# Kernel tuning notes

Measured on AMD Instinct MI355X. Metric: run time of the kernel, lower is better.

The kernel has to match this reference:

```python
import jax, jax.numpy as jnp
import numpy as np

B, H, W, C = 32, 56, 56, 384
WS, SHIFT, HEADS = 7, 3, 12
HIDDEN = 4 * C
N = WS * WS
HEAD_DIM = C // HEADS
SCALE = HEAD_DIM ** -0.5
EPS = 1e-5


def _rel_index(w):
    coords = np.stack(np.meshgrid(np.arange(w), np.arange(w), indexing='ij'))  # [2,w,w]
    cf = coords.reshape(2, -1)                      # [2, w*w]
    rel = (cf[:, :, None] - cf[:, None, :]).transpose(1, 2, 0)  # [N,N,2]
    rel[:, :, 0] += w - 1
    rel[:, :, 1] += w - 1
    rel[:, :, 0] *= 2 * w - 1
    return rel.sum(-1)                              # [N,N] int

REL_IDX = jnp.asarray(_rel_index(WS))


def _layernorm(x, g, b):
    mu = jnp.mean(x, -1, keepdims=True)
    var = jnp.var(x, -1, keepdims=True)
    return (x - mu) * jax.lax.rsqrt(var + EPS) * g + b


def setup_inputs() -> dict:
    key = jax.random.key(0)
    ks = jax.random.split(key, 10)
    s = 0.02
    return {
        'x': jax.random.normal(ks[0], (B, H * W, C), jnp.float32),
        'norm1_g': jnp.ones((C,), jnp.float32),
        'norm1_b': jnp.zeros((C,), jnp.float32),
        'qkv_w': jax.random.normal(ks[1], (C, 3 * C), jnp.float32) * s,
        'qkv_b': jnp.zeros((3 * C,), jnp.float32),
        'rel_bias': jax.random.normal(ks[2], ((2 * WS - 1) ** 2, HEADS), jnp.float32) * s,
        'proj_w': jax.random.normal(ks[3], (C, C), jnp.float32) * s,
        'proj_b': jnp.zeros((C,), jnp.float32),
        'norm2_g': jnp.ones((C,), jnp.float32),
        'norm2_b': jnp.zeros((C,), jnp.float32),
        'fc1_w': jax.random.normal(ks[4], (C, HIDDEN), jnp.float32) * s,
        'fc1_b': jnp.zeros((HIDDEN,), jnp.float32),
        'fc2_w': jax.random.normal(ks[5], (HIDDEN, C), jnp.float32) * s,
        'fc2_b': jnp.zeros((C,), jnp.float32),
    }


def reference(x, norm1_g, norm1_b, qkv_w, qkv_b, rel_bias, proj_w, proj_b,
              norm2_g, norm2_b, fc1_w, fc1_b, fc2_w, fc2_b):
    shortcut = x
    h = _layernorm(x, norm1_g, norm1_b).reshape(B, H, W, C)
    # shifted windows (H,W divisible by WS -> no padding)
    h = jnp.roll(h, (-SHIFT, -SHIFT), axis=(1, 2))
    nH, nW = H // WS, W // WS
    # window partition: [B*nH*nW, N, C]
    win = h.reshape(B, nH, WS, nW, WS, C).transpose(0, 1, 3, 2, 4, 5).reshape(-1, N, C)
    # window attention (source passes mask=None unconditionally)
    qkv = (win @ qkv_w + qkv_b).reshape(-1, N, 3, HEADS, HEAD_DIM)
    q, k, v = [qkv[:, :, i].transpose(0, 2, 1, 3) for i in range(3)]  # [Bw,h,N,d]
    attn = jnp.einsum('bhnd,bhmd->bhnm', q * SCALE, k)
    bias = rel_bias[REL_IDX.reshape(-1)].reshape(N, N, HEADS).transpose(2, 0, 1)
    attn = jax.nn.softmax(attn + bias[None], axis=-1)
    out = jnp.einsum('bhnm,bhmd->bhnd', attn, v).transpose(0, 2, 1, 3).reshape(-1, N, C)
    out = out @ proj_w + proj_b
    # window reverse + unshift
    h = out.reshape(B, nH, nW, WS, WS, C).transpose(0, 1, 3, 2, 4, 5).reshape(B, H, W, C)
    h = jnp.roll(h, (SHIFT, SHIFT), axis=(1, 2)).reshape(B, H * W, C)
    x = shortcut + h
    # MLP
    m = _layernorm(x, norm2_g, norm2_b)
    m = jax.nn.gelu(m @ fc1_w + fc1_b, approximate=False) @ fc2_w + fc2_b
    return x + m
```

## Files before the change

kernel.cpp:

```cpp
#include <hip/hip_runtime.h>
#include <hip/hip_bf16.h>
#include <math.h>

using bf = __hip_bfloat16;
typedef unsigned short u16;
typedef __attribute__((ext_vector_type(8))) unsigned short us8;
typedef __attribute__((ext_vector_type(8))) __bf16 bf16x8;
typedef __attribute__((ext_vector_type(4))) float f32x4;

static constexpr int kC    = 384;
static constexpr int kHid  = 1536;
static constexpr int kHeads= 12;
static constexpr int kN    = 49;
static constexpr float kScale = 0.17677669529663687f;
static constexpr int kWinsTot = 2048;
static constexpr int kRowsTot = kWinsTot * kN;

__device__ __forceinline__ float b2f(bf v){ return __bfloat162float(v); }
__device__ __forceinline__ bf    f2b(float v){ return __float2bfloat16(v); }
__device__ __forceinline__ float ldf(const float* p){ return *p; }
__device__ __forceinline__ float ldf(const bf* p){ return b2f(*p); }

__device__ __forceinline__ float gelu_f(float v){
  float v2 = v*v;
  float y  = v * (0.7978845608f + 0.0356774081f*v2);
  float e  = __builtin_amdgcn_exp2f(y * 2.885390082f);
  float r  = __builtin_amdgcn_rcpf(1.f + e);
  return v - v*r;
}

__device__ __forceinline__ void gload16(const void* g, void* l){
  __builtin_amdgcn_global_load_lds(
      (const __attribute__((address_space(1))) void*)g,
      (__attribute__((address_space(3))) void*)l, 16, 0, 0);
}

__global__ void tr_k(const float* __restrict__ in, bf* __restrict__ out, int K, int N){
  int i = blockIdx.x*256 + threadIdx.x;
  if (i < K*N){ int k = i / N, n = i - k*N; out[(size_t)n*K + k] = f2b(in[i]); }
}

template<int GATHER, typename TIN>
__global__ __launch_bounds__(256) void ln_k(const TIN* __restrict__ x, const float* __restrict__ g,
                                            const float* __restrict__ be, bf* __restrict__ out,
                                            int winbase){
  int wv = threadIdx.x >> 6, lane = threadIdx.x & 63;
  int lr = blockIdx.x*4 + wv;
  const TIN* src;
  if constexpr (GATHER){
    int win = lr / kN, n = lr - win*kN;
    int gw = winbase + win;
    int b = gw >> 6, rem = gw & 63, wh = rem >> 3, ww = rem & 7;
    int ih = n / 7, iw = n - ih*7;
    int h0 = (wh*7 + ih + 3) % 56;
    int w0 = (ww*7 + iw + 3) % 56;
    src = x + ((size_t)b*3136 + h0*56 + w0) * kC;
  } else {
    src = x + (size_t)lr * kC;
  }
  float vals[6]; float s = 0.f, sq = 0.f;
  #pragma unroll
  for (int j = 0; j < 6; ++j){ float f = ldf(src + j*64 + lane); vals[j] = f; s += f; sq += f*f; }
  #pragma unroll
  for (int o = 32; o > 0; o >>= 1){ s += __shfl_down(s, o); sq += __shfl_down(sq, o); }
  s = __shfl(s, 0); sq = __shfl(sq, 0);
  float mean = s * (1.f/384.f);
  float var  = sq * (1.f/384.f) - mean*mean;
  float rstd = rsqrtf(var + 1e-5f);
  bf* dst = out + (size_t)lr * kC;
  #pragma unroll
  for (int j = 0; j < 6; ++j){
    int c = j*64 + lane;
    dst[c] = f2b((vals[j]-mean)*rstd*g[c] + be[c]);
  }
}

template<int EPI, int ALT = 0>
__global__ __launch_bounds__(256, 3) void gemm_k(const bf* __restrict__ A, const bf* __restrict__ Wt,
                                                 const float* __restrict__ bias, int K, int nbn,
                                                 bf* o0, bf* o1, bf* o2,
                                                 float* fo, const void* res, int aux){
  __shared__ char smem[49152];
  u16 (*sA)[4096] = (u16(*)[4096])smem;
  u16 (*sB)[4096] = (u16(*)[4096])(smem + 24576);
  int nwg = gridDim.x, id = blockIdx.x;
  int q = nwg >> 3, r = nwg & 7, xcd = id & 7, off = id >> 3;
  int swz = (xcd < r ? xcd*(q+1) : r*(q+1) + (xcd-r)*q) + off;
  int bm = (swz / nbn) << 7, bn = (swz % nbn) << 7;

  int t = threadIdx.x, lane = t & 63, wv = t >> 6;
  int scol = ((lane & 3) ^ ((lane >> 3) & 3)) * 8;
  const u16* Ag = (const u16*)A  + (size_t)(bm + wv*32 + (lane >> 2))*K + scol;
  const u16* Bg = (const u16*)Wt + (size_t)(bn + wv*32 + (lane >> 2))*K + scol;
  size_t rstep = (size_t)16 * K;
  int l0 = wv*32*32;

  int wr = wv >> 1, wc = wv & 1, lr = lane & 15, lk = lane >> 4;
  int runit = lk ^ ((lr >> 1) & 3);
  int ro = (wr*64 + lr)*32 + runit*8;
  int co = (wc*64 + lr)*32 + runit*8;
  f32x4 acc[4][4];
  #pragma unroll
  for (int i = 0; i < 4; ++i)
    #pragma unroll
    for (int j = 0; j < 4; ++j) acc[i][j] = (f32x4){0.f,0.f,0.f,0.f};

  int nst = K >> 5;
  #define STG(tt, b) { \
    const u16* ag_ = Ag + (size_t)(tt)*32; const u16* bg_ = Bg + (size_t)(tt)*32; \
    gload16(ag_,         &sA[b][l0]);       gload16(ag_ + rstep, &sA[b][l0 + 512]); \
    gload16(bg_,         &sB[b][l0]);       gload16(bg_ + rstep, &sB[b][l0 + 512]); }
  #define STEP(b, tt) { \
    if ((tt) + 2 < nst)      { asm volatile("s_waitcnt vmcnt(8)" ::: "memory"); } \
    else if ((tt) + 1 < nst) { asm volatile("s_waitcnt vmcnt(4)" ::: "memory"); } \
    else                     { asm volatile("s_waitcnt vmcnt(0)" ::: "memory"); } \
    __builtin_amdgcn_s_barrier(); \
    bf16x8 af[4], bfr[4]; \
    _Pragma("unroll") \
    for (int mi = 0; mi < 4; ++mi) af[mi]  = __builtin_bit_cast(bf16x8, *(const us8*)&sA[b][ro + mi*512]); \
    _Pragma("unroll") \
    for (int ni = 0; ni < 4; ++ni) bfr[ni] = __builtin_bit_cast(bf16x8, *(const us8*)&sB[b][co + ni*512]); \
    __builtin_amdgcn_s_setprio(1); \
    _Pragma("unroll") \
    for (int mi = 0; mi < 4; ++mi) \
      _Pragma("unroll") \
      for (int ni = 0; ni < 4; ++ni) \
        acc[mi][ni] = __builtin_amdgcn_mfma_f32_16x16x32_bf16(af[mi], bfr[ni], acc[mi][ni], 0, 0, 0); \
    __builtin_amdgcn_s_setprio(0); \
    asm volatile("s_waitcnt lgkmcnt(0)" ::: "memory"); \
    __builtin_amdgcn_s_barrier(); \
    if ((tt) + 3 < nst) STG((tt) + 3, b); }

  STG(0, 0); STG(1, 1); STG(2, 2);
  for (int tt = 0; tt < nst; tt += 3){
    STEP(0, tt); STEP(1, tt + 1); STEP(2, tt + 2);
  }
  #undef STEP
  #undef STG

  float* tl = (float*)smem + wv*1088;
  float bs[4];
  #pragma unroll
  for (int ni = 0; ni < 4; ++ni) bs[ni] = bias[bn + wc*64 + ni*16 + lr];
  int rrow = lane >> 2, cb = (lane & 3) * 16;
  int colg = bn + wc*64 + cb;
  #pragma unroll
  for (int mi = 0; mi < 4; ++mi){
    #pragma unroll
    for (int ni = 0; ni < 4; ++ni)
      #pragma unroll
      for (int r2 = 0; r2 < 4; ++r2)
        tl[(lk*4 + r2)*68 + ni*16 + lr] = acc[mi][ni][r2] + bs[ni];
    float vals[16];
    #pragma unroll
    for (int j = 0; j < 16; ++j) vals[j] = tl[rrow*68 + cb + j];
    int row = bm + wr*64 + mi*16 + rrow;
    if constexpr (EPI == 0){
      int which = colg / kC; int cc = colg - which*kC; int hd = cc >> 5, d0 = cc & 31;
      int win = row / kN, n = row - win*kN;
      size_t po = (size_t)(win*kHeads + hd)*2048 + n*32 + d0;
      float sc = which == 0 ? kScale : 1.f;
      bf* dst = which == 0 ? o0 : (which == 1 ? o1 : o2);
      us8 p0, p1;
      #pragma unroll
      for (int j = 0; j < 8; ++j){
        p0[j] = __builtin_bit_cast(u16, f2b(vals[j]   * sc));
        p1[j] = __builtin_bit_cast(u16, f2b(vals[j+8] * sc));
      }
      *(us8*)((u16*)dst + po)     = p0;
      *(us8*)((u16*)dst + po + 8) = p1;
    } else if constexpr (EPI == 1){
      int win = row / kN, n = row - win*kN;
      int gw = aux + win;
      int b = gw >> 6, rem = gw & 63, wh = rem >> 3, ww = rem & 7;
      int ih = n / 7, iw = n - ih*7;
      int h0 = (wh*7 + ih + 3) % 56;
      int w0 = (ww*7 + iw + 3) % 56;
      size_t base = ((size_t)b*3136 + h0*56 + w0)*kC + colg;
      const float* xr = (const float*)res;
      #pragma unroll
      for (int q4 = 0; q4 < 4; ++q4){
        f32x4 rv = *(const f32x4*)(xr + base + q4*4);
        #pragma unroll
        for (int j = 0; j < 4; ++j) vals[q4*4 + j] += rv[j];
      }
      if constexpr (ALT){
        us8 p0, p1;
        #pragma unroll
        for (int j = 0; j < 8; ++j){
          p0[j] = __builtin_bit_cast(u16, f2b(vals[j]));
          p1[j] = __builtin_bit_cast(u16, f2b(vals[j+8]));
        }
        *(us8*)((u16*)o0 + base)     = p0;
        *(us8*)((u16*)o0 + base + 8) = p1;
      } else {
        #pragma unroll
        for (int q4 = 0; q4 < 4; ++q4)
          *(f32x4*)(fo + base + q4*4) = (f32x4){vals[q4*4], vals[q4*4+1], vals[q4*4+2], vals[q4*4+3]};
      }
    } else if constexpr (EPI == 2){
      size_t base = (size_t)row*kHid + colg;
      us8 p0, p1;
      #pragma unroll
      for (int j = 0; j < 16; ++j){
        float v = gelu_f(vals[j]);
        if (j < 8) p0[j] = __builtin_bit_cast(u16, f2b(v));
        else       p1[j-8] = __builtin_bit_cast(u16, f2b(v));
      }
      *(us8*)((u16*)o0 + base)     = p0;
      *(us8*)((u16*)o0 + base + 8) = p1;
    } else {
      size_t base = (size_t)row*kC + colg;
      if constexpr (ALT){
        const u16* xb = (const u16*)res;
        us8 r0 = *(const us8*)(xb + base), r1 = *(const us8*)(xb + base + 8);
        #pragma unroll
        for (int j = 0; j < 8; ++j){
          vals[j]   += b2f(__builtin_bit_cast(bf, (u16)r0[j]));
          vals[j+8] += b2f(__builtin_bit_cast(bf, (u16)r1[j]));
        }
      } else {
        const float* xr = (const float*)res;
        #pragma unroll
        for (int q4 = 0; q4 < 4; ++q4){
          f32x4 rv = *(const f32x4*)(xr + base + q4*4);
          #pragma unroll
          for (int j = 0; j < 4; ++j) vals[q4*4 + j] += rv[j];
        }
      }
      #pragma unroll
      for (int q4 = 0; q4 < 4; ++q4)
        *(f32x4*)(fo + base + q4*4) = (f32x4){vals[q4*4], vals[q4*4+1], vals[q4*4+2], vals[q4*4+3]};
    }
  }
}

__global__ __launch_bounds__(256) void attn_k(const bf* __restrict__ qq, const bf* __restrict__ kk,
                                              const bf* __restrict__ vv, const float* __restrict__ relb,
                                              bf* __restrict__ out){
  __shared__ float rbs[169*kHeads];
  __shared__ u16 plds[4][64*64];
  int t = threadIdx.x, wv = t >> 6, l = t & 63;
  for (int i = t; i < 169*kHeads; i += 256) rbs[i] = relb[i];

  int bid = blockIdx.x*4 + wv, lw = bid / kHeads, h = bid - lw*kHeads;
  const u16* qp = (const u16*)qq + (size_t)bid*2048;
  const u16* kp = (const u16*)kk + (size_t)bid*2048;
  const u16* vp = (const u16*)vv + (size_t)bid*2048;
  int fr = l & 15, fk = l >> 4;

  bf16x8 qf[4], kf[4];
  #pragma unroll
  for (int ti = 0; ti < 4; ++ti){
    qf[ti] = __builtin_bit_cast(bf16x8, *(const us8*)(qp + (ti*16 + fr)*32 + fk*8));
    kf[ti] = __builtin_bit_cast(bf16x8, *(const us8*)(kp + (ti*16 + fr)*32 + fk*8));
  }
  f32x4 s[4][4];
  #pragma unroll
  for (int i = 0; i < 4; ++i)
    #pragma unroll
    for (int j = 0; j < 4; ++j) s[i][j] = (f32x4){0.f,0.f,0.f,0.f};
  #pragma unroll
  for (int ti = 0; ti < 4; ++ti)
    #pragma unroll
    for (int tj = 0; tj < 4; ++tj)
      s[ti][tj] = __builtin_amdgcn_mfma_f32_16x16x32_bf16(qf[ti], kf[tj], s[ti][tj], 0, 0, 0);
  __syncthreads();

  int kh[4], kw[4], cvalid[4];
  #pragma unroll
  for (int tj = 0; tj < 4; ++tj){
    int c = tj*16 + fr;
    kh[tj] = c / 7; kw[tj] = c - kh[tj]*7; cvalid[tj] = c < kN;
  }
  #pragma unroll
  for (int ti = 0; ti < 4; ++ti){
    #pragma unroll
    for (int reg = 0; reg < 4; ++reg){
      int R = ti*16 + fk*4 + reg;
      int Rc = R < kN ? R : kN-1;
      int ih = Rc / 7, iw = Rc - ih*7;
      float v[4];
      #pragma unroll
      for (int tj = 0; tj < 4; ++tj){
        float b = rbs[((ih - kh[tj] + 6)*13 + (iw - kw[tj] + 6))*kHeads + h];
        v[tj] = cvalid[tj] ? s[ti][tj][reg] + b : -1e30f;
      }
      float m = fmaxf(fmaxf(v[0], v[1]), fmaxf(v[2], v[3]));
      #pragma unroll
      for (int msk = 1; msk < 16; msk <<= 1) m = fmaxf(m, __shfl_xor(m, msk));
      float e0 = __expf(v[0]-m), e1 = __expf(v[1]-m), e2 = __expf(v[2]-m), e3 = __expf(v[3]-m);
      float sum = (e0+e1) + (e2+e3);
      #pragma unroll
      for (int msk = 1; msk < 16; msk <<= 1) sum += __shfl_xor(sum, msk);
      float inv = 1.f / sum;
      s[ti][0][reg] = e0*inv; s[ti][1][reg] = e1*inv;
      s[ti][2][reg] = e2*inv; s[ti][3][reg] = e3*inv;
    }
  }
  u16* P = plds[wv];
  #pragma unroll
  for (int ti = 0; ti < 4; ++ti)
    #pragma unroll
    for (int tj = 0; tj < 4; ++tj)
      #pragma unroll
      for (int reg = 0; reg < 4; ++reg){
        int R = ti*16 + fk*4 + reg, c = tj*16 + fr;
        P[R*64 + (((c>>3) ^ (R&7)) << 3) + (c&7)] = __builtin_bit_cast(u16, f2b(s[ti][tj][reg]));
      }
  f32x4 o[4][2];
  #pragma unroll
  for (int i = 0; i < 4; ++i){ o[i][0] = (f32x4){0.f,0.f,0.f,0.f}; o[i][1] = (f32x4){0.f,0.f,0.f,0.f}; }
  #pragma unroll
  for (int ks = 0; ks < 2; ++ks){
    bf16x8 vf[2];
    #pragma unroll
    for (int tdj = 0; tdj < 2; ++tdj){
      us8 tmp;
      #pragma unroll
      for (int j = 0; j < 8; ++j)
        tmp[j] = vp[(ks*32 + fk*8 + j)*32 + tdj*16 + fr];
      vf[tdj] = __builtin_bit_cast(bf16x8, tmp);
    }
    #pragma unroll
    for (int ti = 0; ti < 4; ++ti){
      bf16x8 af = __builtin_bit_cast(bf16x8, *(const us8*)&P[(ti*16 + fr)*64 + (((ks*4 + fk) ^ (fr&7)) << 3)]);
      #pragma unroll
      for (int tdj = 0; tdj < 2; ++tdj)
        o[ti][tdj] = __builtin_amdgcn_mfma_f32_16x16x32_bf16(af, vf[tdj], o[ti][tdj], 0, 0, 0);
    }
  }
  #pragma unroll
  for (int ti = 0; ti < 4; ++ti)
    #pragma unroll
    for (int reg = 0; reg < 4; ++reg){
      int R = ti*16 + fk*4 + reg;
      if (R < kN){
        bf* op = out + ((size_t)lw*kN + R)*kC + h*32;
        #pragma unroll
        for (int tdj = 0; tdj < 2; ++tdj)
          op[tdj*16 + fr] = f2b(o[ti][tdj][reg]);
      }
    }
}

extern "C" void kernel_launch(void* const* d_in, const int* in_sizes, int n_in,
                              void* d_out, int out_size, void* d_ws, size_t ws_size,
                              hipStream_t stream){
  (void)in_sizes; (void)n_in; (void)out_size;
  const float* x     = (const float*)d_in[0];
  const float* n1g   = (const float*)d_in[1];
  const float* n1b   = (const float*)d_in[2];
  const float* qkvw  = (const float*)d_in[3];
  const float* qkvb  = (const float*)d_in[4];
  const float* relb  = (const float*)d_in[5];
  const float* projw = (const float*)d_in[6];
  const float* projb = (const float*)d_in[7];
  const float* n2g   = (const float*)d_in[8];
  const float* n2b   = (const float*)d_in[9];
  const float* fc1w  = (const float*)d_in[10];
  const float* fc1b  = (const float*)d_in[11];
  const float* fc2w  = (const float*)d_in[12];
  const float* fc2b  = (const float*)d_in[13];
  float* out = (float*)d_out;
  char* w = (char*)d_ws;

  const size_t WINB_F = 77070336;
  const size_t BIGB_F = 308281344;
  const size_t WTSB   = 3538944;
  const size_t planeF = (size_t)kWinsTot*kHeads*2048;
  const size_t NEED_M = WINB_F + BIGB_F + WTSB + WINB_F;

  if (ws_size >= NEED_M){
    bf* winbuf = (bf*)w;
    bf* big    = (bf*)(w + WINB_F);
    bf* wts    = (bf*)(w + WINB_F + BIGB_F);
    bf* x1b    = (bf*)(w + WINB_F + BIGB_F + WTSB);
    bf* qkvwt  = wts;
    bf* projwt = qkvwt + 442368;
    bf* fc1wt  = projwt + 147456;
    bf* fc2wt  = fc1wt + 589824;
    bf* qb = big; bf* kb = big + planeF; bf* vb = big + 2*planeF;

    tr_k<<<dim3((442368+255)/256), 256, 0, stream>>>(qkvw,  qkvwt, 384, 1152);
    tr_k<<<dim3((147456+255)/256), 256, 0, stream>>>(projw, projwt, 384, 384);
    tr_k<<<dim3((589824+255)/256), 256, 0, stream>>>(fc1w,  fc1wt, 384, 1536);
    tr_k<<<dim3((589824+255)/256), 256, 0, stream>>>(fc2w,  fc2wt, 1536, 384);

    ln_k<1, float><<<kRowsTot/4, 256, 0, stream>>>(x, n1g, n1b, winbuf, 0);
    gemm_k<0><<<784*9, 256, 0, stream>>>(winbuf, qkvwt, qkvb, 384, 9,
                                         qb, kb, vb, nullptr, nullptr, 0);
    attn_k<<<kWinsTot*kHeads/4, 256, 0, stream>>>(qb, kb, vb, relb, winbuf);
    gemm_k<1,1><<<784*3, 256, 0, stream>>>(winbuf, projwt, projb, 384, 3,
                                           x1b, nullptr, nullptr, nullptr, x, 0);
    ln_k<0, bf><<<kRowsTot/4, 256, 0, stream>>>(x1b, n2g, n2b, winbuf, 0);
    gemm_k<2><<<784*12, 256, 0, stream>>>(winbuf, fc1wt, fc1b, 384, 12,
                                          big, nullptr, nullptr, nullptr, nullptr, 0);
    gemm_k<3,1><<<784*3, 256, 0, stream>>>(big, fc2wt, fc2b, 1536, 3,
                                           nullptr, nullptr, nullptr, out, x1b, 0);
  } else {
    const int cw = 512, crows = cw*kN;
    const size_t WINB = 19267584, BIGB = 77070336;
    const size_t planeC = (size_t)cw*kHeads*2048;
    bf* winbuf = (bf*)w;
    bf* big    = (bf*)(w + WINB);
    bf* wts    = (bf*)(w + WINB + BIGB);
    bf* qkvwt  = wts;
    bf* projwt = qkvwt + 442368;
    bf* fc1wt  = projwt + 147456;
    bf* fc2wt  = fc1wt + 589824;
    bf* qb = big; bf* kb = big + planeC; bf* vb = big + 2*planeC;

    tr_k<<<dim3((442368+255)/256), 256, 0, stream>>>(qkvw,  qkvwt, 384, 1152);
    tr_k<<<dim3((147456+255)/256), 256, 0, stream>>>(projw, projwt, 384, 384);
    tr_k<<<dim3((589824+255)/256), 256, 0, stream>>>(fc1w,  fc1wt, 384, 1536);
    tr_k<<<dim3((589824+255)/256), 256, 0, stream>>>(fc2w,  fc2wt, 1536, 384);

    for (int c = 0; c < 4; ++c){
      int winbase = c * cw;
      ln_k<1, float><<<crows/4, 256, 0, stream>>>(x, n1g, n1b, winbuf, winbase);
      gemm_k<0><<<196*9, 256, 0, stream>>>(winbuf, qkvwt, qkvb, 384, 9,
                                           qb, kb, vb, nullptr, nullptr, 0);
      attn_k<<<cw*kHeads/4, 256, 0, stream>>>(qb, kb, vb, relb, winbuf);
      gemm_k<1,0><<<196*3, 256, 0, stream>>>(winbuf, projwt, projb, 384, 3,
                                             nullptr, nullptr, nullptr, out, x, winbase);
    }
    for (int c = 0; c < 4; ++c){
      float* xr = out + (size_t)c * crows * kC;
      ln_k<0, float><<<crows/4, 256, 0, stream>>>(xr, n2g, n2b, winbuf, 0);
      gemm_k<2><<<196*12, 256, 0, stream>>>(winbuf, fc1wt, fc1b, 384, 12,
                                            big, nullptr, nullptr, nullptr, nullptr, 0);
      gemm_k<3,0><<<196*3, 256, 0, stream>>>(big, fc2wt, fc2b, 1536, 3,
                                             nullptr, nullptr, nullptr, xr, xr, 0);
    }
  }
}
```

Before: 838.5 us.

## Process the fast path in two window chunks to shrink intermediate buffers

The full-workspace path now runs the whole layer pipeline (LN1, QKV GEMM, attention, proj, LN2, FC1, FC2) as two chunks of 1024 windows instead of one pass over all 2048. This halves the window and hidden-activation scratch buffers, so each stage's intermediates are more likely to stay resident in the large last-level cache between kernels rather than going to HBM. It also lowers the workspace needed to take this path. The cost is twice as many kernel launches and half-sized grids per launch.

```diff
diff --git a/kernel.cpp b/kernel.cpp
--- a/kernel.cpp
+++ b/kernel.cpp
@@ -13,8 +13,6 @@
 static constexpr int kHeads= 12;
 static constexpr int kN    = 49;
 static constexpr float kScale = 0.17677669529663687f;
-static constexpr int kWinsTot = 2048;
-static constexpr int kRowsTot = kWinsTot * kN;
 
 __device__ __forceinline__ float b2f(bf v){ return __bfloat162float(v); }
 __device__ __forceinline__ bf    f2b(float v){ return __float2bfloat16(v); }
@@ -365,43 +363,51 @@
   float* out = (float*)d_out;
   char* w = (char*)d_ws;
 
-  const size_t WINB_F = 77070336;
-  const size_t BIGB_F = 308281344;
-  const size_t WTSB   = 3538944;
-  const size_t planeF = (size_t)kWinsTot*kHeads*2048;
-  const size_t NEED_M = WINB_F + BIGB_F + WTSB + WINB_F;
-
-  if (ws_size >= NEED_M){
+  const size_t WTSB = 3538944;
+
+  const int cw = 1024, crows = cw*kN;
+  const size_t planeC = (size_t)cw*kHeads*2048;
+  const size_t WINB_C = (size_t)crows*kC*2;
+  const size_t BIGB_C = (size_t)crows*kHid*2;
+  const size_t X1B    = (size_t)2*crows*kC*2;
+  const size_t NEED   = WINB_C + BIGB_C + WTSB + X1B;
+
+  if (ws_size >= NEED){
     bf* winbuf = (bf*)w;
-    bf* big    = (bf*)(w + WINB_F);
-    bf* wts    = (bf*)(w + WINB_F + BIGB_F);
-    bf* x1b    = (bf*)(w + WINB_F + BIGB_F + WTSB);
+    bf* big    = (bf*)(w + WINB_C);
+    bf* wts    = (bf*)(w + WINB_C + BIGB_C);
+    bf* x1b    = (bf*)(w + WINB_C + BIGB_C + WTSB);
     bf* qkvwt  = wts;
     bf* projwt = qkvwt + 442368;
     bf* fc1wt  = projwt + 147456;
     bf* fc2wt  = fc1wt + 589824;
-    bf* qb = big; bf* kb = big + planeF; bf* vb = big + 2*planeF;
+    bf* qb = big; bf* kb = big + planeC; bf* vb = big + 2*planeC;
 
     tr_k<<<dim3((442368+255)/256), 256, 0, stream>>>(qkvw,  qkvwt, 384, 1152);
     tr_k<<<dim3((147456+255)/256), 256, 0, stream>>>(projw, projwt, 384, 384);
     tr_k<<<dim3((589824+255)/256), 256, 0, stream>>>(fc1w,  fc1wt, 384, 1536);
     tr_k<<<dim3((589824+255)/256), 256, 0, stream>>>(fc2w,  fc2wt, 1536, 384);
 
-    ln_k<1, float><<<kRowsTot/4, 256, 0, stream>>>(x, n1g, n1b, winbuf, 0);
-    gemm_k<0><<<784*9, 256, 0, stream>>>(winbuf, qkvwt, qkvb, 384, 9,
-                                         qb, kb, vb, nullptr, nullptr, 0);
-    attn_k<<<kWinsTot*kHeads/4, 256, 0, stream>>>(qb, kb, vb, relb, winbuf);
-    gemm_k<1,1><<<784*3, 256, 0, stream>>>(winbuf, projwt, projb, 384, 3,
-                                           x1b, nullptr, nullptr, nullptr, x, 0);
-    ln_k<0, bf><<<kRowsTot/4, 256, 0, stream>>>(x1b, n2g, n2b, winbuf, 0);
-    gemm_k<2><<<784*12, 256, 0, stream>>>(winbuf, fc1wt, fc1b, 384, 12,
-                                          big, nullptr, nullptr, nullptr, nullptr, 0);
-    gemm_k<3,1><<<784*3, 256, 0, stream>>>(big, fc2wt, fc2b, 1536, 3,
-                                           nullptr, nullptr, nullptr, out, x1b, 0);
+    for (int c = 0; c < 2; ++c){
+      int winbase = c * cw;
+      size_t roff = (size_t)c * crows;
+      ln_k<1, float><<<crows/4, 256, 0, stream>>>(x, n1g, n1b, winbuf, winbase);
+      gemm_k<0><<<392*9, 256, 0, stream>>>(winbuf, qkvwt, qkvb, 384, 9,
+                                           qb, kb, vb, nullptr, nullptr, 0);
+      attn_k<<<cw*kHeads/4, 256, 0, stream>>>(qb, kb, vb, relb, winbuf);
+      gemm_k<1,1><<<392*3, 256, 0, stream>>>(winbuf, projwt, projb, 384, 3,
+                                             x1b, nullptr, nullptr, nullptr, x, winbase);
+      ln_k<0, bf><<<crows/4, 256, 0, stream>>>(x1b + roff*kC, n2g, n2b, winbuf, 0);
+      gemm_k<2><<<392*12, 256, 0, stream>>>(winbuf, fc1wt, fc1b, 384, 12,
+                                            big, nullptr, nullptr, nullptr, nullptr, 0);
+      gemm_k<3,1><<<392*3, 256, 0, stream>>>(big, fc2wt, fc2b, 1536, 3,
+                                             nullptr, nullptr, nullptr,
+                                             out + roff*kC, x1b + roff*kC, 0);
+    }
   } else {
-    const int cw = 512, crows = cw*kN;
+    const int cw4 = 512, crows4 = cw4*kN;
     const size_t WINB = 19267584, BIGB = 77070336;
-    const size_t planeC = (size_t)cw*kHeads*2048;
+    const size_t planeC4 = (size_t)cw4*kHeads*2048;
     bf* winbuf = (bf*)w;
     bf* big    = (bf*)(w + WINB);
     bf* wts    = (bf*)(w + WINB + BIGB);
@@ -409,7 +415,7 @@
     bf* projwt = qkvwt + 442368;
     bf* fc1wt  = projwt + 147456;
     bf* fc2wt  = fc1wt + 589824;
-    bf* qb = big; bf* kb = big + planeC; bf* vb = big + 2*planeC;
+    bf* qb = big; bf* kb = big + planeC4; bf* vb = big + 2*planeC4;
 
     tr_k<<<dim3((442368+255)/256), 256, 0, stream>>>(qkvw,  qkvwt, 384, 1152);
     tr_k<<<dim3((147456+255)/256), 256, 0, stream>>>(projw, projwt, 384, 384);
@@ -417,17 +423,17 @@
     tr_k<<<dim3((589824+255)/256), 256, 0, stream>>>(fc2w,  fc2wt, 1536, 384);
 
     for (int c = 0; c < 4; ++c){
-      int winbase = c * cw;
-      ln_k<1, float><<<crows/4, 256, 0, stream>>>(x, n1g, n1b, winbuf, winbase);
+      int winbase = c * cw4;
+      ln_k<1, float><<<crows4/4, 256, 0, stream>>>(x, n1g, n1b, winbuf, winbase);
       gemm_k<0><<<196*9, 256, 0, stream>>>(winbuf, qkvwt, qkvb, 384, 9,
                                            qb, kb, vb, nullptr, nullptr, 0);
-      attn_k<<<cw*kHeads/4, 256, 0, stream>>>(qb, kb, vb, relb, winbuf);
+      attn_k<<<cw4*kHeads/4, 256, 0, stream>>>(qb, kb, vb, relb, winbuf);
       gemm_k<1,0><<<196*3, 256, 0, stream>>>(winbuf, projwt, projb, 384, 3,
                                              nullptr, nullptr, nullptr, out, x, winbase);
     }
     for (int c = 0; c < 4; ++c){
-      float* xr = out + (size_t)c * crows * kC;
-      ln_k<0, float><<<crows/4, 256, 0, stream>>>(xr, n2g, n2b, winbuf, 0);
+      float* xr = out + (size_t)c * crows4 * kC;
+      ln_k<0, float><<<crows4/4, 256, 0, stream>>>(xr, n2g, n2b, winbuf, 0);
       gemm_k<2><<<196*12, 256, 0, stream>>>(winbuf, fc1wt, fc1b, 384, 12,
                                             big, nullptr, nullptr, nullptr, nullptr, 0);
       gemm_k<3,0><<<196*3, 256, 0, stream>>>(big, fc2wt, fc2b, 1536, 3,
```

Result: faster. 818.4 us (-2.4%).
